# Optimization experiments

Hardware: AMD Instinct MI355X
Metric: run time of the kernel (lower is better)

## Reference

```python
import jax, jax.numpy as jnp
import numpy as np

N_ATOMS = 512
N_SAMPLES = 2 ** 15  # 32768
N_ITER = 64


def time_domain_to_real(x):
    # rfft then concat(real, imag) along last dim -> length 2*(N//2+1)
    s = jnp.fft.rfft(x, axis=-1)
    return jnp.concatenate([s.real, s.imag], axis=-1)


def real_to_time_domain(x):
    half = x.shape[-1] // 2
    c = x[..., :half] + 1j * x[..., half:]
    return jnp.fft.irfft(c, axis=-1)  # n = 2*(half-1) = N_SAMPLES


def setup_inputs() -> dict:
    key = jax.random.key(0)
    k1, k2 = jax.random.split(key)
    x = jax.random.normal(k1, (64, 1, N_SAMPLES), dtype=jnp.float32)
    # learned atoms, initialized exactly as in Model.__init__
    env = jnp.linspace(1.0, 0.0, N_SAMPLES, dtype=jnp.float32) ** 12
    atoms_td = jax.random.uniform(k2, (1, N_ATOMS, N_SAMPLES), dtype=jnp.float32,
                                  minval=-0.01, maxval=0.01) * env[None, None, :]
    atoms = time_domain_to_real(atoms_td)  # (1, N_ATOMS, 32770)
    return {"x": x, "atoms": atoms}


def reference(x, atoms):
    xr = time_domain_to_real(x)            # (B, 1, L), L = 32770
    an = atoms / jnp.linalg.norm(atoms, axis=-1, keepdims=True)  # unit_norm over last axis
    an = an[0]                             # (A, L)
    res0 = xr[:, 0, :]                     # (B, L)
    rec0 = jnp.zeros_like(res0)

    def step(carry, _):
        res, rec = carry
        # sum(atoms * residual, -1) == dot products -> avoid (B,A,L) intermediate
        dots = jnp.einsum('bl,al->ba', res, an)      # (B, A)
        idx = jnp.argmax(dots, axis=1)               # (B,)
        best = an[idx] * res                         # take_along_dim(corr) == atoms[idx]*res
        return (res - best, rec + best), None

    (res, rec), _ = jax.lax.scan(step, (res0, rec0), None, length=N_ITER)
    reconstruction = real_to_time_domain(rec[:, None, :])  # (B, 1, N_SAMPLES)
    return reconstruction, res[:, None, :]
```

## Files before the change

### kernel.cpp

```cpp
#include <hip/hip_runtime.h>
#include <math.h>

#define NSAMP 32768
#define MH    16384
#define LFREQ 32770
#define NRE   16385
#define NB    64
#define NA    512
#define NITER 64
#define RSTR  32772

#define KPS    33280
#define NSL    64
#define USLICE 8
#define NCH    4097

typedef __attribute__((ext_vector_type(8))) short bf16x8;
typedef __attribute__((ext_vector_type(8))) unsigned short u16x8;
typedef __attribute__((ext_vector_type(4))) float f32x4;

__device__ __forceinline__ int rev4_14(int v) {
  unsigned r = __brev((unsigned)v) >> 18;
  r = ((r & 0x1555u) << 1) | ((r >> 1) & 0x1555u);
  return (int)r;
}

__device__ __forceinline__ unsigned short f2bf(float f) {
  unsigned u = __float_as_uint(f);
  u = (u + 0x7fffu + ((u >> 16) & 1u)) >> 16;
  return (unsigned short)u;
}
__device__ __forceinline__ float bf2f(unsigned short h) {
  return __uint_as_float(((unsigned)h) << 16);
}

__device__ __forceinline__ float2 cmul(float2 a, float2 b) {
  return make_float2(a.x * b.x - a.y * b.y, a.x * b.y + a.y * b.x);
}

__global__ __launch_bounds__(1024) void fft_fwd_kernel(const float* __restrict__ x,
                                                       float* __restrict__ res0) {
  extern __shared__ float2 s[];
  const int b = blockIdx.x, t = threadIdx.x;
  const float2* xrow = (const float2*)(x + (size_t)b * NSAMP);
  for (int m = t; m < MH; m += 1024) s[m] = xrow[rev4_14(m)];
  __syncthreads();
  for (int st = 0; st < 7; ++st) {
    const int q = 1 << (2 * st);
    const float fac = 6.283185307179586f / (float)(4 * q);
    for (int j = t; j < MH / 4; j += 1024) {
      const int blk = j >> (2 * st), pos = j & (q - 1);
      const int i0 = (blk << (2 * st + 2)) + pos;
      float sn, cs; __sincosf(fac * (float)pos, &sn, &cs);
      const float2 w1 = make_float2(cs, -sn);
      const float2 w2 = cmul(w1, w1);
      const float2 w3 = cmul(w2, w1);
      const float2 a0 = s[i0], a1 = s[i0 + q], a2 = s[i0 + 2 * q], a3 = s[i0 + 3 * q];
      const float2 x1 = cmul(w1, a1), x2 = cmul(w2, a2), x3 = cmul(w3, a3);
      const float2 s0 = make_float2(a0.x + x2.x, a0.y + x2.y);
      const float2 s1 = make_float2(a0.x - x2.x, a0.y - x2.y);
      const float2 t0 = make_float2(x1.x + x3.x, x1.y + x3.y);
      const float2 t1 = make_float2(x1.x - x3.x, x1.y - x3.y);
      s[i0]         = make_float2(s0.x + t0.x, s0.y + t0.y);
      s[i0 + q]     = make_float2(s1.x + t1.y, s1.y - t1.x);
      s[i0 + 2 * q] = make_float2(s0.x - t0.x, s0.y - t0.y);
      s[i0 + 3 * q] = make_float2(s1.x - t1.y, s1.y + t1.x);
    }
    __syncthreads();
  }
  float* rr = res0 + (size_t)b * RSTR;
  const float fac2 = 6.283185307179586f / (float)NSAMP;
  for (int k = t; k < MH; k += 1024) {
    if (k == 0) {
      const float2 z0 = s[0];
      rr[0] = z0.x + z0.y;      rr[NRE] = 0.f;
      rr[MH] = z0.x - z0.y;     rr[NRE + MH] = 0.f;
    } else {
      const float2 zk = s[k], zm = s[MH - k];
      const float xer = 0.5f * (zk.x + zm.x), xei = 0.5f * (zk.y - zm.y);
      const float p = 0.5f * (zk.y + zm.y);
      const float q = -0.5f * (zk.x - zm.x);
      float sn, cs; __sincosf(fac2 * (float)k, &sn, &cs);
      rr[k]       = xer + cs * p + sn * q;
      rr[NRE + k] = xei + cs * q - sn * p;
    }
  }
}

__global__ __launch_bounds__(1024) void fft_inv_kernel(const float* __restrict__ res0,
                                                       const float* __restrict__ res,
                                                       float* __restrict__ out) {
  extern __shared__ float2 s[];
  const int b = blockIdx.x, t = threadIdx.x;
  const float* r0r = res0 + (size_t)b * RSTR;
  const float* rr = res + (size_t)b * RSTR;
  const float fac2 = 6.283185307179586f / (float)NSAMP;
  for (int m = t; m < MH; m += 1024) {
    const int k = rev4_14(m);
    float2 z;
    if (k == 0) {
      const float a0 = r0r[0] - rr[0], aM = r0r[MH] - rr[MH];
      z = make_float2(0.5f * (a0 + aM), 0.5f * (a0 - aM));
    } else {
      const float xr_ = r0r[k] - rr[k],           xi_ = r0r[NRE + k] - rr[NRE + k];
      const float mr  = r0r[MH - k] - rr[MH - k], mi  = r0r[NRE + MH - k] - rr[NRE + MH - k];
      const float xer = 0.5f * (xr_ + mr), xei = 0.5f * (xi_ - mi);
      const float er  = 0.5f * (xr_ - mr), ei  = 0.5f * (xi_ + mi);
      float sn, cs; __sincosf(fac2 * (float)k, &sn, &cs);
      const float xor_ = cs * er - sn * ei;
      const float xoi  = cs * ei + sn * er;
      z = make_float2(xer - xoi, xei + xor_);
    }
    s[m] = z;
  }
  __syncthreads();
  for (int st = 0; st < 7; ++st) {
    const int q = 1 << (2 * st);
    const float fac = 6.283185307179586f / (float)(4 * q);
    for (int j = t; j < MH / 4; j += 1024) {
      const int blk = j >> (2 * st), pos = j & (q - 1);
      const int i0 = (blk << (2 * st + 2)) + pos;
      float sn, cs; __sincosf(fac * (float)pos, &sn, &cs);
      const float2 w1 = make_float2(cs, sn);
      const float2 w2 = cmul(w1, w1);
      const float2 w3 = cmul(w2, w1);
      const float2 a0 = s[i0], a1 = s[i0 + q], a2 = s[i0 + 2 * q], a3 = s[i0 + 3 * q];
      const float2 x1 = cmul(w1, a1), x2 = cmul(w2, a2), x3 = cmul(w3, a3);
      const float2 s0 = make_float2(a0.x + x2.x, a0.y + x2.y);
      const float2 s1 = make_float2(a0.x - x2.x, a0.y - x2.y);
      const float2 t0 = make_float2(x1.x + x3.x, x1.y + x3.y);
      const float2 t1 = make_float2(x1.x - x3.x, x1.y - x3.y);
      s[i0]         = make_float2(s0.x + t0.x, s0.y + t0.y);
      s[i0 + q]     = make_float2(s1.x - t1.y, s1.y + t1.x);
      s[i0 + 2 * q] = make_float2(s0.x - t0.x, s0.y - t0.y);
      s[i0 + 3 * q] = make_float2(s1.x + t1.y, s1.y - t1.x);
    }
    __syncthreads();
  }
  const float inv = 1.0f / (float)MH;
  float2* orow = (float2*)(out + (size_t)b * NSAMP);
  for (int m = t; m < MH; m += 1024) {
    const float2 z = s[m];
    orow[m] = make_float2(z.x * inv, z.y * inv);
  }
}

__global__ __launch_bounds__(256) void atom_norm_kernel(const float* __restrict__ atoms,
                                                        float* __restrict__ rnorm,
                                                        float* __restrict__ anv) {
  const int a = blockIdx.x, t = threadIdx.x;
  const float2* row2 = (const float2*)(atoms + (size_t)a * LFREQ);
  float ss = 0.f;
  for (int i = t; i < LFREQ / 2; i += 256) {
    const float2 v = row2[i];
    ss += v.x * v.x + v.y * v.y;
  }
  __shared__ float red[256];
  red[t] = ss; __syncthreads();
  for (int st = 128; st > 0; st >>= 1) {
    if (t < st) red[t] += red[t + st];
    __syncthreads();
  }
  if (t == 0) {
    const float rn = 1.0f / sqrtf(red[0]);
    rnorm[a] = rn;
    anv[a] = atoms[(size_t)a * LFREQ + 32768] * rn;
  }
}

__global__ __launch_bounds__(256) void an_bf16_kernel(const float* __restrict__ atoms,
                                                      const float* __restrict__ rnorm,
                                                      unsigned short* __restrict__ anH,
                                                      unsigned short* __restrict__ anL) {
  const int quarter = blockIdx.x;
  const int a = blockIdx.y;
  const int t = threadIdx.x;
  const float rn = rnorm[a];
  const float* row = atoms + (size_t)a * LFREQ;
  unsigned short* hrow = anH + (size_t)a * KPS;
  unsigned short* lrow = anL + (size_t)a * KPS;
  const int c0 = quarter * 1040;
  const int c1 = min(c0 + 1040, KPS / 8);
  for (int c = c0 + t; c < c1; c += 256) {
    const int k0 = c * 8;
    float v[8];
    if (k0 + 8 <= LFREQ) {
      #pragma unroll
      for (int e = 0; e < 4; ++e) {
        const float2 p = *(const float2*)(row + k0 + 2 * e);
        v[2 * e] = p.x; v[2 * e + 1] = p.y;
      }
    } else {
      #pragma unroll
      for (int e = 0; e < 8; ++e) v[e] = (k0 + e < LFREQ) ? row[k0 + e] : 0.f;
    }
    u16x8 hv, lv;
    #pragma unroll
    for (int e = 0; e < 8; ++e) {
      const float sv = v[e] * rn;
      const unsigned short h = f2bf(sv);
      hv[e] = h;
      lv[e] = f2bf(sv - bf2f(h));
    }
    *(u16x8*)(hrow + k0) = hv;
    *(u16x8*)(lrow + k0) = lv;
  }
}

__global__ __launch_bounds__(256) void res_convert_kernel(const float* __restrict__ res0,
                                                          float* __restrict__ res,
                                                          unsigned short* __restrict__ resH,
                                                          unsigned short* __restrict__ resL) {
  const int b = blockIdx.x, t = threadIdx.x;
  const float* row0 = res0 + (size_t)b * RSTR;
  float* rowf = res + (size_t)b * RSTR;
  unsigned short* hrow = resH + (size_t)b * KPS;
  unsigned short* lrow = resL + (size_t)b * KPS;
  for (int c = t; c < KPS / 8; c += 256) {
    const int k0 = c * 8;
    float v[8];
    if (k0 + 8 <= LFREQ) {
      #pragma unroll
      for (int e = 0; e < 2; ++e) {
        const float4 p = *(const float4*)(row0 + k0 + 4 * e);
        v[4 * e] = p.x; v[4 * e + 1] = p.y; v[4 * e + 2] = p.z; v[4 * e + 3] = p.w;
        *(float4*)(rowf + k0 + 4 * e) = p;
      }
    } else {
      #pragma unroll
      for (int e = 0; e < 8; ++e) {
        const int k = k0 + e;
        if (k < LFREQ) { v[e] = row0[k]; rowf[k] = v[e]; }
        else v[e] = 0.f;
      }
    }
    u16x8 hv, lv;
    #pragma unroll
    for (int e = 0; e < 8; ++e) {
      const unsigned short h = f2bf(v[e]);
      hv[e] = h;
      lv[e] = f2bf(v[e] - bf2f(h));
    }
    *(u16x8*)(hrow + k0) = hv;
    *(u16x8*)(lrow + k0) = lv;
  }
}

__global__ __launch_bounds__(256) void dots_mfma_kernel(const unsigned short* __restrict__ resH,
                                                        const unsigned short* __restrict__ resL,
                                                        const unsigned short* __restrict__ anH,
                                                        const unsigned short* __restrict__ anL,
                                                        float* __restrict__ partials) {
  __shared__ char smem[65536];
  const int slice = blockIdx.x;
  const int atile = blockIdx.y;
  const int t = threadIdx.x;
  const int w = t >> 6, l = t & 63;
  const int bh = w >> 1, ah = w & 1;
  const int kc0 = slice * 512;

  const unsigned short* gtab = (w == 0) ? resH : (w == 1) ? resL : (w == 2) ? anH : anL;
  const int rowoff = (w >= 2) ? atile * 64 : 0;
  const int lrow = rowoff + (l & 15);
  const int lkof = (l >> 4) * 8;

  f32x4 acc00 = {0.f,0.f,0.f,0.f}, acc01 = acc00, acc10 = acc00, acc11 = acc00;

#define STAGE(cc, bb)                                                                     \
  {                                                                                       \
    const int kc = kc0 + (cc) * 64;                                                       \
    _Pragma("unroll")                                                                     \
    for (int si = 0; si < 8; ++si) {                                                      \
      const unsigned short* g = gtab + (size_t)(lrow + (si >> 1) * 16) * KPS              \
                                + kc + (si & 1) * 32 + lkof;                              \
      char* d = smem + (bb) * 32768 + w * 8192 + si * 1024;                               \
      __builtin_amdgcn_global_load_lds((const __attribute__((address_space(1))) void*)g,  \
                                       (__attribute__((address_space(3))) void*)d,        \
                                       16, 0, 0);                                         \
    }                                                                                     \
  }

#define COMPUTE(bb)                                                                      \
  {                                                                                       \
    const char* base = smem + (bb) * 32768;                                               \
    _Pragma("unroll")                                                                     \
    for (int kk = 0; kk < 2; ++kk) {                                                      \
      const bf16x8 aH0 = *(const bf16x8*)(base + ((bh * 2 + 0) * 2 + kk) * 1024 + l * 16);\
      const bf16x8 aH1 = *(const bf16x8*)(base + ((bh * 2 + 1) * 2 + kk) * 1024 + l * 16);\
      const bf16x8 aL0 = *(const bf16x8*)(base + 8192 + ((bh * 2 + 0) * 2 + kk) * 1024 + l * 16);\
      const bf16x8 aL1 = *(const bf16x8*)(base + 8192 + ((bh * 2 + 1) * 2 + kk) * 1024 + l * 16);\
      const bf16x8 bH0 = *(const bf16x8*)(base + 16384 + ((ah * 2 + 0) * 2 + kk) * 1024 + l * 16);\
      const bf16x8 bH1 = *(const bf16x8*)(base + 16384 + ((ah * 2 + 1) * 2 + kk) * 1024 + l * 16);\
      const bf16x8 bL0 = *(const bf16x8*)(base + 24576 + ((ah * 2 + 0) * 2 + kk) * 1024 + l * 16);\
      const bf16x8 bL1 = *(const bf16x8*)(base + 24576 + ((ah * 2 + 1) * 2 + kk) * 1024 + l * 16);\
      acc00 = __builtin_amdgcn_mfma_f32_16x16x32_bf16(aH0, bH0, acc00, 0, 0, 0);          \
      acc01 = __builtin_amdgcn_mfma_f32_16x16x32_bf16(aH0, bH1, acc01, 0, 0, 0);          \
      acc10 = __builtin_amdgcn_mfma_f32_16x16x32_bf16(aH1, bH0, acc10, 0, 0, 0);          \
      acc11 = __builtin_amdgcn_mfma_f32_16x16x32_bf16(aH1, bH1, acc11, 0, 0, 0);          \
      acc00 = __builtin_amdgcn_mfma_f32_16x16x32_bf16(aH0, bL0, acc00, 0, 0, 0);          \
      acc01 = __builtin_amdgcn_mfma_f32_16x16x32_bf16(aH0, bL1, acc01, 0, 0, 0);          \
      acc10 = __builtin_amdgcn_mfma_f32_16x16x32_bf16(aH1, bL0, acc10, 0, 0, 0);          \
      acc11 = __builtin_amdgcn_mfma_f32_16x16x32_bf16(aH1, bL1, acc11, 0, 0, 0);          \
      acc00 = __builtin_amdgcn_mfma_f32_16x16x32_bf16(aL0, bH0, acc00, 0, 0, 0);          \
      acc01 = __builtin_amdgcn_mfma_f32_16x16x32_bf16(aL0, bH1, acc01, 0, 0, 0);          \
      acc10 = __builtin_amdgcn_mfma_f32_16x16x32_bf16(aL1, bH0, acc10, 0, 0, 0);          \
      acc11 = __builtin_amdgcn_mfma_f32_16x16x32_bf16(aL1, bH1, acc11, 0, 0, 0);          \
    }                                                                                     \
  }

  STAGE(0, 0);
  #pragma unroll
  for (int c = 0; c < 8; ++c) {
    const int buf = c & 1;
    if (c < 7) {
      STAGE(c + 1, buf ^ 1);
      asm volatile("s_waitcnt vmcnt(8)" ::: "memory");
    } else {
      asm volatile("s_waitcnt vmcnt(0)" ::: "memory");
    }
    __builtin_amdgcn_s_barrier();
    __builtin_amdgcn_sched_barrier(0);
    COMPUTE(buf);
    __builtin_amdgcn_sched_barrier(0);
    __builtin_amdgcn_s_barrier();
  }
#undef STAGE
#undef COMPUTE

  const int brow = bh * 32 + (l >> 4) * 4;
  const int acol = atile * 64 + ah * 32 + (l & 15);
  float* pp = partials + ((size_t)brow * NSL + slice) * NA + acol;
  const size_t bstr = (size_t)NSL * NA;
  #pragma unroll
  for (int e = 0; e < 4; ++e) {
    pp[(size_t)e * bstr]             = acc00[e];
    pp[(size_t)e * bstr + 16]        = acc01[e];
    pp[(size_t)(16 + e) * bstr]      = acc10[e];
    pp[(size_t)(16 + e) * bstr + 16] = acc11[e];
  }
}

__global__ __launch_bounds__(256) void reduce_argmax_kernel(const float* __restrict__ partials,
                                                            const float* __restrict__ res,
                                                            const float* __restrict__ anv,
                                                            int* __restrict__ bestidx) {
  const int b = blockIdx.x, t = threadIdx.x;
  const float* pb = partials + (size_t)b * NSL * NA;
  float d0 = 0.f, d1 = 0.f;
  #pragma unroll 16
  for (int s = 0; s < NSL; ++s) {
    d0 += pb[(size_t)s * NA + t];
    d1 += pb[(size_t)s * NA + t + 256];
  }
  const float rv = res[(size_t)b * RSTR + 32768];
  d0 = fmaf(rv, anv[t], d0);
  d1 = fmaf(rv, anv[t + 256], d1);
  float best = d0; int bi = t;
  if (d1 > best) { best = d1; bi = t + 256; }
  __shared__ float sv[256]; __shared__ int si[256];
  sv[t] = best; si[t] = bi; __syncthreads();
  for (int st = 128; st > 0; st >>= 1) {
    if (t < st) {
      const float v2 = sv[t + st]; const int i2 = si[t + st];
      if (v2 > sv[t] || (v2 == sv[t] && i2 < si[t])) { sv[t] = v2; si[t] = i2; }
    }
    __syncthreads();
  }
  if (t == 0) bestidx[b] = si[0];
}

__global__ __launch_bounds__(256) void update_kernel(float* __restrict__ res,
                                                     const float* __restrict__ atoms,
                                                     const float* __restrict__ rnorm,
                                                     const int* __restrict__ bestidx,
                                                     unsigned short* __restrict__ resH,
                                                     unsigned short* __restrict__ resL,
                                                     float* __restrict__ out2,
                                                     int final_out) {
  const int slice = blockIdx.x;
  const int b = blockIdx.y;
  const int t = threadIdx.x;
  const int idx = bestidx[b];
  const float rn = rnorm[idx];
  const float* arow = atoms + (size_t)idx * LFREQ;
  float* rrow = res + (size_t)b * RSTR;
  unsigned short* hrow = resH + (size_t)b * KPS;
  unsigned short* lrow = resL + (size_t)b * KPS;
  float* orow = out2 + (size_t)b * LFREQ;
  const int c0 = slice * 513;
  const int c1 = min(c0 + 513, NCH);
  for (int c = c0 + t; c < c1; c += 256) {
    const int k0 = c * 8;
    if (k0 + 8 <= LFREQ) {
      float rv[8], av[8];
      #pragma unroll
      for (int e = 0; e < 2; ++e) {
        const float4 q = *(const float4*)(rrow + k0 + 4 * e);
        rv[4 * e] = q.x; rv[4 * e + 1] = q.y; rv[4 * e + 2] = q.z; rv[4 * e + 3] = q.w;
      }
      #pragma unroll
      for (int e = 0; e < 4; ++e) {
        const float2 p = *(const float2*)(arow + k0 + 2 * e);
        av[2 * e] = p.x; av[2 * e + 1] = p.y;
      }
      float nv[8];
      u16x8 hv, lv;
      #pragma unroll
      for (int e = 0; e < 8; ++e) {
        const float bx = av[e] * rn * rv[e];
        nv[e] = rv[e] - bx;
        const unsigned short h = f2bf(nv[e]);
        hv[e] = h;
        lv[e] = f2bf(nv[e] - bf2f(h));
      }
      #pragma unroll
      for (int e = 0; e < 2; ++e)
        *(float4*)(rrow + k0 + 4 * e) = make_float4(nv[4*e], nv[4*e+1], nv[4*e+2], nv[4*e+3]);
      *(u16x8*)(hrow + k0) = hv;
      *(u16x8*)(lrow + k0) = lv;
      if (final_out) {
        #pragma unroll
        for (int e = 0; e < 2; ++e)
          *(float4*)(orow + k0 + 4 * e) = make_float4(nv[4*e], nv[4*e+1], nv[4*e+2], nv[4*e+3]);
      }
    } else {
      for (int e = 0; e < 8; ++e) {
        const int k = k0 + e;
        if (k < LFREQ) {
          const float r = rrow[k], a = arow[k];
          const float bx = a * rn * r;
          const float nx = r - bx;
          rrow[k] = nx;
          const unsigned short h = f2bf(nx);
          hrow[k] = h;
          lrow[k] = f2bf(nx - bf2f(h));
          if (final_out) orow[k] = nx;
        }
      }
    }
  }
}

extern "C" void kernel_launch(void* const* d_in, const int* in_sizes, int n_in,
                              void* d_out, int out_size, void* d_ws, size_t ws_size,
                              hipStream_t stream) {
  const float* x = (const float*)d_in[0];
  const float* atoms = (const float*)d_in[1];
  float* out = (float*)d_out;

  float* res0 = (float*)d_ws;
  float* res = res0 + (size_t)NB * RSTR;
  float* rnorm = res + (size_t)NB * RSTR;
  float* anv = rnorm + NA;
  float* partials = anv + NA;
  int* bestidx = (int*)(partials + (size_t)NB * NSL * NA);
  unsigned short* resH = (unsigned short*)(bestidx + 64);
  unsigned short* resL = resH + (size_t)NB * KPS;
  unsigned short* anH  = resL + (size_t)NB * KPS;
  unsigned short* anL  = anH + (size_t)NA * KPS;

  atom_norm_kernel<<<NA, 256, 0, stream>>>(atoms, rnorm, anv);
  an_bf16_kernel<<<dim3(4, NA), 256, 0, stream>>>(atoms, rnorm, anH, anL);
  fft_fwd_kernel<<<NB, 1024, MH * sizeof(float2), stream>>>(x, res0);
  res_convert_kernel<<<NB, 256, 0, stream>>>(res0, res, resH, resL);

  float* res_out = out + (size_t)NB * NSAMP;
  for (int it = 0; it < NITER; ++it) {
    dots_mfma_kernel<<<dim3(NSL, 8), 256, 0, stream>>>(resH, resL, anH, anL, partials);
    reduce_argmax_kernel<<<NB, 256, 0, stream>>>(partials, res, anv, bestidx);
    update_kernel<<<dim3(USLICE, NB), 256, 0, stream>>>(res, atoms, rnorm, bestidx,
                                                        resH, resL, res_out,
                                                        (it == NITER - 1) ? 1 : 0);
  }

  fft_inv_kernel<<<NB, 1024, MH * sizeof(float2), stream>>>(res0, res, out);
}
```

Before: 2.134 ms.

## Drop fp32 residual; keep residual only as bf16 hi/lo pair

Result: faster. 2.008 ms (-5.9%).

```diff
diff --git a/kernel.cpp b/kernel.cpp
--- a/kernel.cpp
+++ b/kernel.cpp
@@ -39,7 +39,9 @@
 }
 
 __global__ __launch_bounds__(1024) void fft_fwd_kernel(const float* __restrict__ x,
-                                                       float* __restrict__ res0) {
+                                                       float* __restrict__ res0,
+                                                       unsigned short* __restrict__ resH,
+                                                       unsigned short* __restrict__ resL) {
   extern __shared__ float2 s[];
   const int b = blockIdx.x, t = threadIdx.x;
   const float2* xrow = (const float2*)(x + (size_t)b * NSAMP);
@@ -69,41 +71,52 @@
     __syncthreads();
   }
   float* rr = res0 + (size_t)b * RSTR;
+  unsigned short* hrow = resH + (size_t)b * KPS;
+  unsigned short* lrow = resL + (size_t)b * KPS;
   const float fac2 = 6.283185307179586f / (float)NSAMP;
   for (int k = t; k < MH; k += 1024) {
     if (k == 0) {
       const float2 z0 = s[0];
-      rr[0] = z0.x + z0.y;      rr[NRE] = 0.f;
-      rr[MH] = z0.x - z0.y;     rr[NRE + MH] = 0.f;
+      const float dc = z0.x + z0.y, ny = z0.x - z0.y;
+      rr[0] = dc;   rr[NRE] = 0.f;
+      rr[MH] = ny;  rr[NRE + MH] = 0.f;
+      unsigned short h;
+      h = f2bf(dc); hrow[0] = h;  lrow[0] = f2bf(dc - bf2f(h));
+      h = f2bf(ny); hrow[MH] = h; lrow[MH] = f2bf(ny - bf2f(h));
+      hrow[NRE] = 0; lrow[NRE] = 0;
+      hrow[NRE + MH] = 0; lrow[NRE + MH] = 0;
     } else {
       const float2 zk = s[k], zm = s[MH - k];
       const float xer = 0.5f * (zk.x + zm.x), xei = 0.5f * (zk.y - zm.y);
       const float p = 0.5f * (zk.y + zm.y);
       const float q = -0.5f * (zk.x - zm.x);
       float sn, cs; __sincosf(fac2 * (float)k, &sn, &cs);
-      rr[k]       = xer + cs * p + sn * q;
-      rr[NRE + k] = xei + cs * q - sn * p;
-    }
-  }
-}
-
-__global__ __launch_bounds__(1024) void fft_inv_kernel(const float* __restrict__ res0,
-                                                       const float* __restrict__ res,
+      const float vr = xer + cs * p + sn * q;
+      const float vi = xei + cs * q - sn * p;
+      rr[k]       = vr;
+      rr[NRE + k] = vi;
+      unsigned short h;
+      h = f2bf(vr); hrow[k] = h;       lrow[k] = f2bf(vr - bf2f(h));
+      h = f2bf(vi); hrow[NRE + k] = h; lrow[NRE + k] = f2bf(vi - bf2f(h));
+    }
+  }
+}
+
+__global__ __launch_bounds__(1024) void fft_inv_kernel(const float* __restrict__ rec,
                                                        float* __restrict__ out) {
   extern __shared__ float2 s[];
   const int b = blockIdx.x, t = threadIdx.x;
-  const float* r0r = res0 + (size_t)b * RSTR;
-  const float* rr = res + (size_t)b * RSTR;
+  const float* rr = rec + (size_t)b * RSTR;
   const float fac2 = 6.283185307179586f / (float)NSAMP;
   for (int m = t; m < MH; m += 1024) {
     const int k = rev4_14(m);
     float2 z;
     if (k == 0) {
-      const float a0 = r0r[0] - rr[0], aM = r0r[MH] - rr[MH];
+      const float a0 = rr[0], aM = rr[MH];
       z = make_float2(0.5f * (a0 + aM), 0.5f * (a0 - aM));
     } else {
-      const float xr_ = r0r[k] - rr[k],           xi_ = r0r[NRE + k] - rr[NRE + k];
-      const float mr  = r0r[MH - k] - rr[MH - k], mi  = r0r[NRE + MH - k] - rr[NRE + MH - k];
+      const float xr_ = rr[k],       xi_ = rr[NRE + k];
+      const float mr  = rr[MH - k],  mi  = rr[NRE + MH - k];
       const float xer = 0.5f * (xr_ + mr), xei = 0.5f * (xi_ - mi);
       const float er  = 0.5f * (xr_ - mr), ei  = 0.5f * (xi_ + mi);
       float sn, cs; __sincosf(fac2 * (float)k, &sn, &cs);
@@ -201,45 +214,6 @@
       const unsigned short h = f2bf(sv);
       hv[e] = h;
       lv[e] = f2bf(sv - bf2f(h));
-    }
-    *(u16x8*)(hrow + k0) = hv;
-    *(u16x8*)(lrow + k0) = lv;
-  }
-}
-
-__global__ __launch_bounds__(256) void res_convert_kernel(const float* __restrict__ res0,
-                                                          float* __restrict__ res,
-                                                          unsigned short* __restrict__ resH,
-                                                          unsigned short* __restrict__ resL) {
-  const int b = blockIdx.x, t = threadIdx.x;
-  const float* row0 = res0 + (size_t)b * RSTR;
-  float* rowf = res + (size_t)b * RSTR;
-  unsigned short* hrow = resH + (size_t)b * KPS;
-  unsigned short* lrow = resL + (size_t)b * KPS;
-  for (int c = t; c < KPS / 8; c += 256) {
-    const int k0 = c * 8;
-    float v[8];
-    if (k0 + 8 <= LFREQ) {
-      #pragma unroll
-      for (int e = 0; e < 2; ++e) {
-        const float4 p = *(const float4*)(row0 + k0 + 4 * e);
-        v[4 * e] = p.x; v[4 * e + 1] = p.y; v[4 * e + 2] = p.z; v[4 * e + 3] = p.w;
-        *(float4*)(rowf + k0 + 4 * e) = p;
-      }
-    } else {
-      #pragma unroll
-      for (int e = 0; e < 8; ++e) {
-        const int k = k0 + e;
-        if (k < LFREQ) { v[e] = row0[k]; rowf[k] = v[e]; }
-        else v[e] = 0.f;
-      }
-    }
-    u16x8 hv, lv;
-    #pragma unroll
-    for (int e = 0; e < 8; ++e) {
-      const unsigned short h = f2bf(v[e]);
-      hv[e] = h;
-      lv[e] = f2bf(v[e] - bf2f(h));
     }
     *(u16x8*)(hrow + k0) = hv;
     *(u16x8*)(lrow + k0) = lv;
@@ -341,7 +315,8 @@
 }
 
 __global__ __launch_bounds__(256) void reduce_argmax_kernel(const float* __restrict__ partials,
-                                                            const float* __restrict__ res,
+                                                            const unsigned short* __restrict__ resH,
+                                                            const unsigned short* __restrict__ resL,
                                                             const float* __restrict__ anv,
                                                             int* __restrict__ bestidx) {
   const int b = blockIdx.x, t = threadIdx.x;
@@ -352,7 +327,8 @@
     d0 += pb[(size_t)s * NA + t];
     d1 += pb[(size_t)s * NA + t + 256];
   }
-  const float rv = res[(size_t)b * RSTR + 32768];
+  const float rv = bf2f(resH[(size_t)b * KPS + 32768]) +
+                   bf2f(resL[(size_t)b * KPS + 32768]);
   d0 = fmaf(rv, anv[t], d0);
   d1 = fmaf(rv, anv[t + 256], d1);
   float best = d0; int bi = t;
@@ -369,12 +345,13 @@
   if (t == 0) bestidx[b] = si[0];
 }
 
-__global__ __launch_bounds__(256) void update_kernel(float* __restrict__ res,
-                                                     const float* __restrict__ atoms,
+__global__ __launch_bounds__(256) void update_kernel(const float* __restrict__ atoms,
                                                      const float* __restrict__ rnorm,
                                                      const int* __restrict__ bestidx,
                                                      unsigned short* __restrict__ resH,
                                                      unsigned short* __restrict__ resL,
+                                                     const float* __restrict__ res0,
+                                                     float* __restrict__ rec,
                                                      float* __restrict__ out2,
                                                      int final_out) {
   const int slice = blockIdx.x;
@@ -383,21 +360,19 @@
   const int idx = bestidx[b];
   const float rn = rnorm[idx];
   const float* arow = atoms + (size_t)idx * LFREQ;
-  float* rrow = res + (size_t)b * RSTR;
   unsigned short* hrow = resH + (size_t)b * KPS;
   unsigned short* lrow = resL + (size_t)b * KPS;
+  const float* r0row = res0 + (size_t)b * RSTR;
+  float* recrow = rec + (size_t)b * RSTR;
   float* orow = out2 + (size_t)b * LFREQ;
   const int c0 = slice * 513;
   const int c1 = min(c0 + 513, NCH);
   for (int c = c0 + t; c < c1; c += 256) {
     const int k0 = c * 8;
     if (k0 + 8 <= LFREQ) {
-      float rv[8], av[8];
-      #pragma unroll
-      for (int e = 0; e < 2; ++e) {
-        const float4 q = *(const float4*)(rrow + k0 + 4 * e);
-        rv[4 * e] = q.x; rv[4 * e + 1] = q.y; rv[4 * e + 2] = q.z; rv[4 * e + 3] = q.w;
-      }
+      const u16x8 hv0 = *(const u16x8*)(hrow + k0);
+      const u16x8 lv0 = *(const u16x8*)(lrow + k0);
+      float av[8];
       #pragma unroll
       for (int e = 0; e < 4; ++e) {
         const float2 p = *(const float2*)(arow + k0 + 2 * e);
@@ -407,34 +382,38 @@
       u16x8 hv, lv;
       #pragma unroll
       for (int e = 0; e < 8; ++e) {
-        const float bx = av[e] * rn * rv[e];
-        nv[e] = rv[e] - bx;
+        const float r = bf2f(hv0[e]) + bf2f(lv0[e]);
+        const float bx = av[e] * rn * r;
+        nv[e] = r - bx;
         const unsigned short h = f2bf(nv[e]);
         hv[e] = h;
         lv[e] = f2bf(nv[e] - bf2f(h));
       }
-      #pragma unroll
-      for (int e = 0; e < 2; ++e)
-        *(float4*)(rrow + k0 + 4 * e) = make_float4(nv[4*e], nv[4*e+1], nv[4*e+2], nv[4*e+3]);
       *(u16x8*)(hrow + k0) = hv;
       *(u16x8*)(lrow + k0) = lv;
       if (final_out) {
         #pragma unroll
-        for (int e = 0; e < 2; ++e)
+        for (int e = 0; e < 2; ++e) {
+          const float4 r0 = *(const float4*)(r0row + k0 + 4 * e);
           *(float4*)(orow + k0 + 4 * e) = make_float4(nv[4*e], nv[4*e+1], nv[4*e+2], nv[4*e+3]);
+          *(float4*)(recrow + k0 + 4 * e) = make_float4(r0.x - nv[4*e], r0.y - nv[4*e+1],
+                                                       r0.z - nv[4*e+2], r0.w - nv[4*e+3]);
+        }
       }
     } else {
       for (int e = 0; e < 8; ++e) {
         const int k = k0 + e;
         if (k < LFREQ) {
-          const float r = rrow[k], a = arow[k];
-          const float bx = a * rn * r;
+          const float r = bf2f(hrow[k]) + bf2f(lrow[k]);
+          const float bx = arow[k] * rn * r;
           const float nx = r - bx;
-          rrow[k] = nx;
           const unsigned short h = f2bf(nx);
           hrow[k] = h;
           lrow[k] = f2bf(nx - bf2f(h));
-          if (final_out) orow[k] = nx;
+          if (final_out) {
+            orow[k] = nx;
+            recrow[k] = r0row[k] - nx;
+          }
         }
       }
     }
@@ -449,8 +428,8 @@
   float* out = (float*)d_out;
 
   float* res0 = (float*)d_ws;
-  float* res = res0 + (size_t)NB * RSTR;
-  float* rnorm = res + (size_t)NB * RSTR;
+  float* rec = res0 + (size_t)NB * RSTR;
+  float* rnorm = rec + (size_t)NB * RSTR;
   float* anv = rnorm + NA;
   float* partials = anv + NA;
   int* bestidx = (int*)(partials + (size_t)NB * NSL * NA);
@@ -459,19 +438,19 @@
   unsigned short* anH  = resL + (size_t)NB * KPS;
   unsigned short* anL  = anH + (size_t)NA * KPS;
 
+  hipMemsetAsync(resH, 0, (size_t)NB * KPS * sizeof(unsigned short) * 2, stream);
   atom_norm_kernel<<<NA, 256, 0, stream>>>(atoms, rnorm, anv);
   an_bf16_kernel<<<dim3(4, NA), 256, 0, stream>>>(atoms, rnorm, anH, anL);
-  fft_fwd_kernel<<<NB, 1024, MH * sizeof(float2), stream>>>(x, res0);
-  res_convert_kernel<<<NB, 256, 0, stream>>>(res0, res, resH, resL);
+  fft_fwd_kernel<<<NB, 1024, MH * sizeof(float2), stream>>>(x, res0, resH, resL);
 
   float* res_out = out + (size_t)NB * NSAMP;
   for (int it = 0; it < NITER; ++it) {
     dots_mfma_kernel<<<dim3(NSL, 8), 256, 0, stream>>>(resH, resL, anH, anL, partials);
-    reduce_argmax_kernel<<<NB, 256, 0, stream>>>(partials, res, anv, bestidx);
-    update_kernel<<<dim3(USLICE, NB), 256, 0, stream>>>(res, atoms, rnorm, bestidx,
-                                                        resH, resL, res_out,
+    reduce_argmax_kernel<<<NB, 256, 0, stream>>>(partials, resH, resL, anv, bestidx);
+    update_kernel<<<dim3(USLICE, NB), 256, 0, stream>>>(atoms, rnorm, bestidx,
+                                                        resH, resL, res0, rec, res_out,
                                                         (it == NITER - 1) ? 1 : 0);
   }
 
-  fft_inv_kernel<<<NB, 1024, MH * sizeof(float2), stream>>>(res0, res, out);
-}
+  fft_inv_kernel<<<NB, 1024, MH * sizeof(float2), stream>>>(rec, out);
+}
```
